# Performance work log

Hardware: AMD Instinct MI355X
Metric: run time of the kernel (lower is better)

## Reference

```python
import jax, jax.numpy as jnp
import numpy as np

M_STEP = 3  # model_args.m_step
E_STEP = 3  # model_args.e_step


def setup_inputs() -> dict:
    key = jax.random.key(0)
    ks = jax.random.split(key, 8)
    B, N, F = 1024, 11, 512   # batch, num_nodes (=round_id+2), message_size
    H = 512                   # link_hidden_size
    sc = 1.0 / np.sqrt(F)
    rnd = lambda k, shape: (jax.random.normal(k, shape, jnp.float32) * sc)
    return {
        "node_features": jax.random.normal(ks[0], (B, N, F), jnp.float32),
        "W1": rnd(ks[1], (H, F)),
        "b1": jnp.zeros((H,), jnp.float32),
        "W2": rnd(ks[2], (H, H)),
        "b2": jnp.zeros((H,), jnp.float32),
        "w_out": rnd(ks[3], (H,)),
        "b_out": jnp.zeros((), jnp.float32),
        "W_ih": rnd(ks[4], (3 * F, F)),  # GRU input weights (r,z,n), bias=False
        "W_hh": rnd(ks[5], (3 * F, F)),  # GRU hidden weights
    }


def _link_adj(x, W1, b1, W2, b2, w_out, b_out):
    # LinkFunction('graphconvattn'): pairwise node-feature interactions -> 1x1 conv stack -> [B,N,N]
    # x: [B,F,N]
    e = x[:, :, :, None] * x[:, :, None, :]                                  # [B,F,N,N]
    h = jax.nn.relu(jnp.einsum('bfij,gf->bgij', e, W1) + b1[None, :, None, None])
    h = jax.nn.relu(jnp.einsum('bfij,gf->bgij', h, W2) + b2[None, :, None, None])
    return jnp.einsum('bfij,f->bij', h, w_out) + b_out                       # [B,N,N]


def _gru_cell(m, h, W_ih, W_hh):
    # torch nn.GRU cell, bias=False, gate order (r, z, n)
    gi = m @ W_ih.T
    gh = h @ W_hh.T
    ir, iz, inn = jnp.split(gi, 3, axis=-1)
    hr, hz, hn = jnp.split(gh, 3, axis=-1)
    r = jax.nn.sigmoid(ir + hr)
    z = jax.nn.sigmoid(iz + hz)
    n = jnp.tanh(inn + r * hn)
    return (1.0 - z) * n + z * h


def reference(node_features, W1, b1, W2, b2, w_out, b_out, W_ih, W_hh):
    x0 = jnp.transpose(node_features, (0, 2, 1))   # [B,F,N]
    N = x0.shape[2]
    zidx = N - 1                                   # only the question node is updated
    col = x0[:, :, zidx]
    adj = None
    for t in range(M_STEP):
        # pred_node_feats[t]: original features with node z replaced by latest estimate
        pred = x0.at[:, :, zidx].set(col)
        adj = _link_adj(pred, W1, b1, W2, b2, w_out, b_out)
        A = jax.nn.softmax(adj, axis=2)            # softmax over neighbors
        a_z = A[:, zidx, :]                        # [B,N]
        h = pred
        for s in range(E_STEP):
            m_z = jnp.einsum('bj,bfj->bf', a_z, h)             # weighted message
            h_z = _gru_cell(m_z, h[:, :, zidx], W_ih, W_hh)    # GRU update
            h = h.at[:, :, zidx].set(h_z)
        col = h[:, :, zidx]
    # returns (pred_adj_mat from last m-step, final feature of node z)
    return adj, col
```

## Files before the change

kernel.cpp:

```cpp
#include <hip/hip_runtime.h>
#include <hip/hip_bf16.h>
#include <math.h>

#define Bsz 1024
#define Nn  11
#define Ff  512
#define Zi  10
#define G3  1536

#define PEC 65

typedef __attribute__((ext_vector_type(8))) short bfrag;
typedef __attribute__((ext_vector_type(4))) float f32x4;

__device__ __forceinline__ unsigned f2bf(float f) {
    __hip_bfloat16 h = __float2bfloat16(f);
    return (unsigned)*reinterpret_cast<unsigned short*>(&h);
}
__device__ __forceinline__ uint4 pack8(float v0, float v1, float v2, float v3,
                                       float v4, float v5, float v6, float v7) {
    uint4 pk;
    pk.x = f2bf(v0) | (f2bf(v1) << 16);
    pk.y = f2bf(v2) | (f2bf(v3) << 16);
    pk.z = f2bf(v4) | (f2bf(v5) << 16);
    pk.w = f2bf(v6) | (f2bf(v7) << 16);
    return pk;
}
__device__ __forceinline__ void pair_decode(int mode, int p, int& pi, int& pj) {
    if (mode == 0) { int r = p, i = 0; while (r >= Nn - i) { r -= Nn - i; ++i; } pi = i; pj = i + r; }
    else { pi = p; pj = Zi; }
}
__device__ __forceinline__ void gl_lds16(const void* src, void* dst) {
    __builtin_amdgcn_global_load_lds((const __attribute__((address_space(1))) void*)src,
                                     (__attribute__((address_space(3))) void*)dst, 16, 0, 0);
}

__global__ void init_col_kernel(const float* __restrict__ nf, float* __restrict__ col) {
    int idx = blockIdx.x * 256 + threadIdx.x;
    int b = idx >> 9, f = idx & 511;
    col[idx] = nf[(b * Nn + Zi) * Ff + f];
}

__global__ void pack_w_kernel(const float* __restrict__ src,
                              unsigned short* __restrict__ dst, int lgBW) {
    int idx = blockIdx.x * 256 + threadIdx.x;
    int g = idx >> 6, kq = idx & 63;
    int nb = g >> lgBW, gl = g & ((1 << lgBW) - 1);
    const float* s = src + g * Ff + kq * 8;
    float4 a = *(const float4*)s, b = *(const float4*)(s + 4);
    uint4 pk = pack8(a.x, a.y, a.z, a.w, b.x, b.y, b.z, b.w);
    long long dc = (((long long)(nb << 6) + kq) << lgBW) + gl;
    *(uint4*)((char*)dst + dc * 16) = pk;
}

__global__ __launch_bounds__(512, 2) void link_kernel(
    const float* __restrict__ nf, const float* __restrict__ colp,
    const unsigned short* __restrict__ W1p, const float* __restrict__ b1,
    const unsigned short* __restrict__ W2p, const float* __restrict__ b2,
    const float* __restrict__ w_out, const float* __restrict__ b_out,
    float* __restrict__ adj, int mode)
{
    __shared__ __align__(16) char Eb[64 * PEC * 16];
    __shared__ float Pl[8][64];

    const int tid = threadIdx.x;
    const int pr  = blockIdx.x >> 4;
    const int bc  = blockIdx.x & 15;
    int pi, pj; pair_decode(mode, pr, pi, pj);

    const int wid  = tid >> 6;
    const int l    = tid & 63;
    const int lr16 = l & 15;
    const int kq4  = l >> 4;

    const bfrag* W1c = (const bfrag*)W1p;
    const bfrag* W2c = (const bfrag*)W2p;
    const int wcb = wid * 64 + lr16;

    bfrag wb0[4], wb1[4];
    auto loadW = [&](int gs, bfrag* dst) {
        const bfrag* Wc = (gs >= 16) ? W2c : W1c;
        const int base = ((gs & 15) * 4 + kq4) * 512 + wcb;
#pragma unroll
        for (int nt = 0; nt < 4; ++nt) dst[nt] = Wc[base + nt * 16];
    };

    loadW(0, wb0);

    {
        const int row = tid >> 3;
        const int kc  = tid & 7;
        const int b   = bc * 64 + row;
        const float* xi = (pi == Zi) ? (colp + b * Ff) : (nf + (b * Nn + pi) * Ff);
        const float* xj = (pj == Zi) ? (colp + b * Ff) : (nf + (b * Nn + pj) * Ff);
#pragma unroll
        for (int i = 0; i < 8; ++i) {
            const int k0 = kc * 64 + i * 8;
            const int plane = k0 >> 3;
            float4 u0 = *(const float4*)(xi + k0), u1 = *(const float4*)(xi + k0 + 4);
            float4 v0 = *(const float4*)(xj + k0), v1 = *(const float4*)(xj + k0 + 4);
            *(uint4*)(&Eb[(plane * PEC + row) * 16]) =
                pack8(u0.x*v0.x, u0.y*v0.y, u0.z*v0.z, u0.w*v0.w,
                      u1.x*v1.x, u1.y*v1.y, u1.z*v1.z, u1.w*v1.w);
        }
    }
    __syncthreads();

    f32x4 acc[4][4];
#pragma unroll
    for (int mt = 0; mt < 4; ++mt)
#pragma unroll
        for (int nt = 0; nt < 4; ++nt) acc[mt][nt] = (f32x4){0.f, 0.f, 0.f, 0.f};

#define DO_STEP(S, WB) { \
    const int ebase = ((S) & 15) * 4 + kq4; \
    bfrag a0 = *(const bfrag*)(&Eb[(ebase * PEC +      lr16) * 16]); \
    bfrag a1 = *(const bfrag*)(&Eb[(ebase * PEC + 16 + lr16) * 16]); \
    bfrag a2 = *(const bfrag*)(&Eb[(ebase * PEC + 32 + lr16) * 16]); \
    bfrag a3 = *(const bfrag*)(&Eb[(ebase * PEC + 48 + lr16) * 16]); \
    acc[0][0] = __builtin_amdgcn_mfma_f32_16x16x32_bf16(a0, WB[0], acc[0][0], 0, 0, 0); \
    acc[0][1] = __builtin_amdgcn_mfma_f32_16x16x32_bf16(a0, WB[1], acc[0][1], 0, 0, 0); \
    acc[0][2] = __builtin_amdgcn_mfma_f32_16x16x32_bf16(a0, WB[2], acc[0][2], 0, 0, 0); \
    acc[0][3] = __builtin_amdgcn_mfma_f32_16x16x32_bf16(a0, WB[3], acc[0][3], 0, 0, 0); \
    acc[1][0] = __builtin_amdgcn_mfma_f32_16x16x32_bf16(a1, WB[0], acc[1][0], 0, 0, 0); \
    acc[1][1] = __builtin_amdgcn_mfma_f32_16x16x32_bf16(a1, WB[1], acc[1][1], 0, 0, 0); \
    acc[1][2] = __builtin_amdgcn_mfma_f32_16x16x32_bf16(a1, WB[2], acc[1][2], 0, 0, 0); \
    acc[1][3] = __builtin_amdgcn_mfma_f32_16x16x32_bf16(a1, WB[3], acc[1][3], 0, 0, 0); \
    acc[2][0] = __builtin_amdgcn_mfma_f32_16x16x32_bf16(a2, WB[0], acc[2][0], 0, 0, 0); \
    acc[2][1] = __builtin_amdgcn_mfma_f32_16x16x32_bf16(a2, WB[1], acc[2][1], 0, 0, 0); \
    acc[2][2] = __builtin_amdgcn_mfma_f32_16x16x32_bf16(a2, WB[2], acc[2][2], 0, 0, 0); \
    acc[2][3] = __builtin_amdgcn_mfma_f32_16x16x32_bf16(a2, WB[3], acc[2][3], 0, 0, 0); \
    acc[3][0] = __builtin_amdgcn_mfma_f32_16x16x32_bf16(a3, WB[0], acc[3][0], 0, 0, 0); \
    acc[3][1] = __builtin_amdgcn_mfma_f32_16x16x32_bf16(a3, WB[1], acc[3][1], 0, 0, 0); \
    acc[3][2] = __builtin_amdgcn_mfma_f32_16x16x32_bf16(a3, WB[2], acc[3][2], 0, 0, 0); \
    acc[3][3] = __builtin_amdgcn_mfma_f32_16x16x32_bf16(a3, WB[3], acc[3][3], 0, 0, 0); }

#pragma unroll 1
    for (int s2 = 0; s2 < 8; ++s2) {
        const int s = 2 * s2;
        loadW(s + 1, wb1);
        DO_STEP(s, wb0)
        loadW(s + 2, wb0);
        DO_STEP(s + 1, wb1)
    }

    __syncthreads();
    {
#pragma unroll
        for (int nt = 0; nt < 4; ++nt) {
            const int c  = wid * 64 + nt * 16 + lr16;
            const float bv = b1[c];
#pragma unroll
            for (int mt = 0; mt < 4; ++mt)
#pragma unroll
                for (int reg = 0; reg < 4; ++reg) {
                    int row = mt * 16 + kq4 * 4 + reg;
                    float v = fmaxf(acc[mt][nt][reg] + bv, 0.f);
                    *(unsigned short*)(&Eb[((c >> 3) * PEC + row) * 16 + (c & 7) * 2]) =
                        (unsigned short)f2bf(v);
                }
        }
#pragma unroll
        for (int mt = 0; mt < 4; ++mt)
#pragma unroll
            for (int nt = 0; nt < 4; ++nt) acc[mt][nt] = (f32x4){0.f, 0.f, 0.f, 0.f};
    }
    __syncthreads();

#pragma unroll 1
    for (int s2 = 0; s2 < 8; ++s2) {
        const int s = 16 + 2 * s2;
        loadW(s + 1, wb1);
        DO_STEP(s, wb0)
        if (s2 < 7) loadW(s + 2, wb0);
        DO_STEP(s + 1, wb1)
    }
#undef DO_STEP

    {
        float rs[4][4];
#pragma unroll
        for (int mt = 0; mt < 4; ++mt)
#pragma unroll
            for (int reg = 0; reg < 4; ++reg) rs[mt][reg] = 0.f;
#pragma unroll
        for (int nt = 0; nt < 4; ++nt) {
            const int c  = wid * 64 + nt * 16 + lr16;
            const float bv = b2[c];
            const float wv = w_out[c];
#pragma unroll
            for (int mt = 0; mt < 4; ++mt)
#pragma unroll
                for (int reg = 0; reg < 4; ++reg)
                    rs[mt][reg] += fmaxf(acc[mt][nt][reg] + bv, 0.f) * wv;
        }
#pragma unroll
        for (int off = 1; off < 16; off <<= 1)
#pragma unroll
            for (int mt = 0; mt < 4; ++mt)
#pragma unroll
                for (int reg = 0; reg < 4; ++reg)
                    rs[mt][reg] += __shfl_xor(rs[mt][reg], off);
        if (lr16 == 0) {
#pragma unroll
            for (int mt = 0; mt < 4; ++mt)
#pragma unroll
                for (int reg = 0; reg < 4; ++reg) {
                    int row = mt * 16 + kq4 * 4 + reg;
                    Pl[wid][row] = rs[mt][reg];
                }
        }
    }
    __syncthreads();
    if (tid < 64) {
        float v = b_out[0];
#pragma unroll
        for (int w = 0; w < 8; ++w) v += Pl[w][tid];
        int b = bc * 64 + tid;
        adj[b * (Nn * Nn) + pi * Nn + pj] = v;
        if (pi != pj) adj[b * (Nn * Nn) + pj * Nn + pi] = v;
    }
}

__global__ void softmax_az_kernel(const float* __restrict__ adj, float* __restrict__ a_z) {
    int b = blockIdx.x * 256 + threadIdx.x;
    if (b >= Bsz) return;
    const float* row = adj + b * (Nn * Nn) + Zi * Nn;
    float mx = row[0];
#pragma unroll
    for (int j = 1; j < Nn; ++j) mx = fmaxf(mx, row[j]);
    float e[Nn]; float s = 0.f;
#pragma unroll
    for (int j = 0; j < Nn; ++j) { e[j] = expf(row[j] - mx); s += e[j]; }
    float inv = 1.f / s;
#pragma unroll
    for (int j = 0; j < Nn; ++j) a_z[b * Nn + j] = e[j] * inv;
}

__global__ void mzpack_kernel(const float* __restrict__ nf, const float* __restrict__ a_z,
                              const float* __restrict__ col,
                              unsigned short* __restrict__ m_zp,
                              unsigned short* __restrict__ colbf) {
    int idx = blockIdx.x * 256 + threadIdx.x;
    int b = idx >> 6, kq = idx & 63;
    const float* az = a_z + b * Nn;
    const int f0 = kq * 8;
    float4 c0 = *(const float4*)(col + b * Ff + f0);
    float4 c1 = *(const float4*)(col + b * Ff + f0 + 4);
    float az10 = az[Zi];
    float s0 = az10 * c0.x, s1 = az10 * c0.y, s2 = az10 * c0.z, s3 = az10 * c0.w;
    float s4 = az10 * c1.x, s5 = az10 * c1.y, s6 = az10 * c1.z, s7 = az10 * c1.w;
#pragma unroll
    for (int j = 0; j < Nn - 1; ++j) {
        float aj = az[j];
        const float* p = nf + (b * Nn + j) * Ff + f0;
        float4 n0 = *(const float4*)p, n1 = *(const float4*)(p + 4);
        s0 += aj * n0.x; s1 += aj * n0.y; s2 += aj * n0.z; s3 += aj * n0.w;
        s4 += aj * n1.x; s5 += aj * n1.y; s6 += aj * n1.z; s7 += aj * n1.w;
    }
    long long dc = (((long long)(b >> 6) * 64 + kq) << 6) + (b & 63);
    *(uint4*)((char*)m_zp + dc * 16)  = pack8(s0, s1, s2, s3, s4, s5, s6, s7);
    *(uint4*)((char*)colbf + dc * 16) = pack8(c0.x, c0.y, c0.z, c0.w, c1.x, c1.y, c1.z, c1.w);
}

__global__ __launch_bounds__(256, 2) void gates_kernel(
    const unsigned short* __restrict__ m_zp, const unsigned short* __restrict__ colbf,
    const unsigned short* __restrict__ Wihp, const unsigned short* __restrict__ Whhp,
    float* __restrict__ gi, float* __restrict__ gh)
{
    __shared__ __align__(16) char Ab[64 * 64 * 16];

    const int xb = blockIdx.x, bc = blockIdx.y, tid = threadIdx.x;
    const bool isGi = xb < 6;
    const int nbase = (isGi ? xb : xb - 6) * 256;
    const unsigned short* Ap = isGi ? m_zp : colbf;
    const unsigned short* Wp = isGi ? Wihp : Whhp;
    float* C = isGi ? gi : gh;

    const int wid  = tid >> 6;
    const int l    = tid & 63;
    const int lr16 = l & 15;
    const int kq4  = l >> 4;

    const bfrag* Wc = (const bfrag*)Wp;
    const int wcb = ((nbase >> 9) << 15) + (nbase & 511) + wid * 64 + lr16;

    bfrag wb0[4], wb1[4];
    auto loadW = [&](int s, bfrag* dst) {
        const int base = wcb + (s * 4 + kq4) * 512;
#pragma unroll
        for (int nt = 0; nt < 4; ++nt) dst[nt] = Wc[base + nt * 16];
    };

    loadW(0, wb0);

#pragma unroll
    for (int i = 0; i < 16; ++i) {
        int cb = i * 256 + wid * 64;
        gl_lds16(Ap + ((long long)bc * 4096 + cb + l) * 8, (char*)Ab + cb * 16);
    }
    __syncthreads();

    f32x4 acc[4][4];
#pragma unroll
    for (int mt = 0; mt < 4; ++mt)
#pragma unroll
        for (int nt = 0; nt < 4; ++nt) acc[mt][nt] = (f32x4){0.f, 0.f, 0.f, 0.f};

#define DO_STEPG(S, WB) { \
    const int ebase = (S) * 4 + kq4; \
    bfrag a0 = *(const bfrag*)(&Ab[(ebase * 64 +      lr16) * 16]); \
    bfrag a1 = *(const bfrag*)(&Ab[(ebase * 64 + 16 + lr16) * 16]); \
    bfrag a2 = *(const bfrag*)(&Ab[(ebase * 64 + 32 + lr16) * 16]); \
    bfrag a3 = *(const bfrag*)(&Ab[(ebase * 64 + 48 + lr16) * 16]); \
    acc[0][0] = __builtin_amdgcn_mfma_f32_16x16x32_bf16(a0, WB[0], acc[0][0], 0, 0, 0); \
    acc[0][1] = __builtin_amdgcn_mfma_f32_16x16x32_bf16(a0, WB[1], acc[0][1], 0, 0, 0); \
    acc[0][2] = __builtin_amdgcn_mfma_f32_16x16x32_bf16(a0, WB[2], acc[0][2], 0, 0, 0); \
    acc[0][3] = __builtin_amdgcn_mfma_f32_16x16x32_bf16(a0, WB[3], acc[0][3], 0, 0, 0); \
    acc[1][0] = __builtin_amdgcn_mfma_f32_16x16x32_bf16(a1, WB[0], acc[1][0], 0, 0, 0); \
    acc[1][1] = __builtin_amdgcn_mfma_f32_16x16x32_bf16(a1, WB[1], acc[1][1], 0, 0, 0); \
    acc[1][2] = __builtin_amdgcn_mfma_f32_16x16x32_bf16(a1, WB[2], acc[1][2], 0, 0, 0); \
    acc[1][3] = __builtin_amdgcn_mfma_f32_16x16x32_bf16(a1, WB[3], acc[1][3], 0, 0, 0); \
    acc[2][0] = __builtin_amdgcn_mfma_f32_16x16x32_bf16(a2, WB[0], acc[2][0], 0, 0, 0); \
    acc[2][1] = __builtin_amdgcn_mfma_f32_16x16x32_bf16(a2, WB[1], acc[2][1], 0, 0, 0); \
    acc[2][2] = __builtin_amdgcn_mfma_f32_16x16x32_bf16(a2, WB[2], acc[2][2], 0, 0, 0); \
    acc[2][3] = __builtin_amdgcn_mfma_f32_16x16x32_bf16(a2, WB[3], acc[2][3], 0, 0, 0); \
    acc[3][0] = __builtin_amdgcn_mfma_f32_16x16x32_bf16(a3, WB[0], acc[3][0], 0, 0, 0); \
    acc[3][1] = __builtin_amdgcn_mfma_f32_16x16x32_bf16(a3, WB[1], acc[3][1], 0, 0, 0); \
    acc[3][2] = __builtin_amdgcn_mfma_f32_16x16x32_bf16(a3, WB[2], acc[3][2], 0, 0, 0); \
    acc[3][3] = __builtin_amdgcn_mfma_f32_16x16x32_bf16(a3, WB[3], acc[3][3], 0, 0, 0); }

#pragma unroll 1
    for (int s2 = 0; s2 < 8; ++s2) {
        const int s = 2 * s2;
        loadW(s + 1, wb1);
        DO_STEPG(s, wb0)
        if (s2 < 7) loadW(s + 2, wb0);
        DO_STEPG(s + 1, wb1)
    }
#undef DO_STEPG

#pragma unroll
    for (int nt = 0; nt < 4; ++nt) {
        const int c = nbase + wid * 64 + nt * 16 + lr16;
#pragma unroll
        for (int mt = 0; mt < 4; ++mt)
#pragma unroll
            for (int reg = 0; reg < 4; ++reg) {
                int row = mt * 16 + kq4 * 4 + reg;
                C[(bc * 64 + row) * G3 + c] = acc[mt][nt][reg];
            }
    }
}

__global__ void gru_kernel(const float* __restrict__ gi, const float* __restrict__ gh,
                           float* __restrict__ col) {
    int idx = blockIdx.x * 256 + threadIdx.x;
    int b = idx >> 7, f = (idx & 127) * 4;
    const float* gib = gi + b * G3;
    const float* ghb = gh + b * G3;
    float4 ir = *(const float4*)(gib + f);
    float4 iz = *(const float4*)(gib + Ff + f);
    float4 in = *(const float4*)(gib + 2 * Ff + f);
    float4 hr = *(const float4*)(ghb + f);
    float4 hz = *(const float4*)(ghb + Ff + f);
    float4 hn = *(const float4*)(ghb + 2 * Ff + f);
    float4 h  = *(const float4*)(col + b * Ff + f);
    float4 o;
#define GRU1(c) { \
    float r = 1.f / (1.f + expf(-(ir.c + hr.c))); \
    float z = 1.f / (1.f + expf(-(iz.c + hz.c))); \
    float n = tanhf(in.c + r * hn.c); \
    o.c = (1.f - z) * n + z * h.c; }
    GRU1(x) GRU1(y) GRU1(z) GRU1(w)
#undef GRU1
    *(float4*)(col + b * Ff + f) = o;
}

extern "C" void kernel_launch(void* const* d_in, const int* in_sizes, int n_in,
                              void* d_out, int out_size, void* d_ws, size_t ws_size,
                              hipStream_t stream) {
    const float* nf    = (const float*)d_in[0];
    const float* W1    = (const float*)d_in[1];
    const float* b1    = (const float*)d_in[2];
    const float* W2    = (const float*)d_in[3];
    const float* b2    = (const float*)d_in[4];
    const float* w_out = (const float*)d_in[5];
    const float* b_out = (const float*)d_in[6];
    const float* W_ih  = (const float*)d_in[7];
    const float* W_hh  = (const float*)d_in[8];

    float* adj = (float*)d_out;
    float* col = adj + Bsz * Nn * Nn;

    unsigned short* W1p   = (unsigned short*)d_ws;
    unsigned short* W2p   = W1p + Ff * Ff;
    unsigned short* Wihp  = W2p + Ff * Ff;
    unsigned short* Whhp  = Wihp + G3 * Ff;
    float* a_z            = (float*)(Whhp + G3 * Ff);
    unsigned short* m_zp  = (unsigned short*)(a_z + 16384);
    unsigned short* colbf = m_zp + Bsz * Ff;
    float* gi             = (float*)(colbf + Bsz * Ff);
    float* gh             = gi + Bsz * G3;

    init_col_kernel<<<(Bsz * Ff) / 256, 256, 0, stream>>>(nf, col);
    pack_w_kernel<<<(Ff * 64) / 256, 256, 0, stream>>>(W1, W1p, 9);
    pack_w_kernel<<<(Ff * 64) / 256, 256, 0, stream>>>(W2, W2p, 9);
    pack_w_kernel<<<(G3 * 64) / 256, 256, 0, stream>>>(W_ih, Wihp, 9);
    pack_w_kernel<<<(G3 * 64) / 256, 256, 0, stream>>>(W_hh, Whhp, 9);

    for (int t = 0; t < 3; ++t) {
        const int mode   = (t == 0) ? 0 : 1;
        const int npairs = (t == 0) ? 66 : 11;

        link_kernel<<<npairs * 16, 512, 0, stream>>>(nf, col, W1p, b1, W2p, b2,
                                                     w_out, b_out, adj, mode);
        softmax_az_kernel<<<Bsz / 256, 256, 0, stream>>>(adj, a_z);

        for (int s = 0; s < 3; ++s) {
            mzpack_kernel<<<(Bsz * 64) / 256, 256, 0, stream>>>(nf, a_z, col, m_zp, colbf);
            gates_kernel<<<dim3(12, 16), 256, 0, stream>>>(m_zp, colbf, Wihp, Whhp, gi, gh);
            gru_kernel<<<(Bsz * Ff) / 4 / 256, 256, 0, stream>>>(gi, gh, col);
        }
    }
}
```

Before: 364.4 us.

## Double link-kernel batch tile to 128 rows and triple-buffer gates weight loads

The link kernel now processes 128 batch rows per block instead of 64, so each loaded weight fragment feeds twice as many MFMAs and the grid is halved. This doubles accumulator registers and LDS use, and the launch bound of two blocks per SM may cause spills. The gates kernel gets padded LDS rows (PEC) to reduce bank conflicts and a three-deep weight prefetch rotation. A W2 prefetch is also moved out of the phase boundary, with weight indices clamped.

After: 435.7 us. 19.6% more time.

```diff
diff --git a/kernel.cpp b/kernel.cpp
--- a/kernel.cpp
+++ b/kernel.cpp
@@ -8,7 +8,8 @@
 #define Zi  10
 #define G3  1536
 
-#define PEC 65
+#define PEC  66
+#define PEL  130
 
 typedef __attribute__((ext_vector_type(8))) short bfrag;
 typedef __attribute__((ext_vector_type(4))) float f32x4;
@@ -60,12 +61,12 @@
     const float* __restrict__ w_out, const float* __restrict__ b_out,
     float* __restrict__ adj, int mode)
 {
-    __shared__ __align__(16) char Eb[64 * PEC * 16];
-    __shared__ float Pl[8][64];
+    __shared__ __align__(16) char Eb[64 * PEL * 16];
+    __shared__ float Pl[8][128];
 
     const int tid = threadIdx.x;
-    const int pr  = blockIdx.x >> 4;
-    const int bc  = blockIdx.x & 15;
+    const int pr  = blockIdx.x >> 3;
+    const int bc  = blockIdx.x & 7;
     int pi, pj; pair_decode(mode, pr, pi, pj);
 
     const int wid  = tid >> 6;
@@ -79,6 +80,7 @@
 
     bfrag wb0[4], wb1[4];
     auto loadW = [&](int gs, bfrag* dst) {
+        if (gs > 31) gs = 31;
         const bfrag* Wc = (gs >= 16) ? W2c : W1c;
         const int base = ((gs & 15) * 4 + kq4) * 512 + wcb;
 #pragma unroll
@@ -88,52 +90,40 @@
     loadW(0, wb0);
 
     {
-        const int row = tid >> 3;
-        const int kc  = tid & 7;
-        const int b   = bc * 64 + row;
+        const int row = tid >> 2;
+        const int kc  = tid & 3;
+        const int b   = bc * 128 + row;
         const float* xi = (pi == Zi) ? (colp + b * Ff) : (nf + (b * Nn + pi) * Ff);
         const float* xj = (pj == Zi) ? (colp + b * Ff) : (nf + (b * Nn + pj) * Ff);
 #pragma unroll
-        for (int i = 0; i < 8; ++i) {
-            const int k0 = kc * 64 + i * 8;
+        for (int i = 0; i < 16; ++i) {
+            const int k0 = kc * 128 + i * 8;
             const int plane = k0 >> 3;
             float4 u0 = *(const float4*)(xi + k0), u1 = *(const float4*)(xi + k0 + 4);
             float4 v0 = *(const float4*)(xj + k0), v1 = *(const float4*)(xj + k0 + 4);
-            *(uint4*)(&Eb[(plane * PEC + row) * 16]) =
+            *(uint4*)(&Eb[(plane * PEL + row) * 16]) =
                 pack8(u0.x*v0.x, u0.y*v0.y, u0.z*v0.z, u0.w*v0.w,
                       u1.x*v1.x, u1.y*v1.y, u1.z*v1.z, u1.w*v1.w);
         }
     }
     __syncthreads();
 
-    f32x4 acc[4][4];
-#pragma unroll
-    for (int mt = 0; mt < 4; ++mt)
+    f32x4 acc[8][4];
+#pragma unroll
+    for (int mt = 0; mt < 8; ++mt)
 #pragma unroll
         for (int nt = 0; nt < 4; ++nt) acc[mt][nt] = (f32x4){0.f, 0.f, 0.f, 0.f};
 
 #define DO_STEP(S, WB) { \
     const int ebase = ((S) & 15) * 4 + kq4; \
-    bfrag a0 = *(const bfrag*)(&Eb[(ebase * PEC +      lr16) * 16]); \
-    bfrag a1 = *(const bfrag*)(&Eb[(ebase * PEC + 16 + lr16) * 16]); \
-    bfrag a2 = *(const bfrag*)(&Eb[(ebase * PEC + 32 + lr16) * 16]); \
-    bfrag a3 = *(const bfrag*)(&Eb[(ebase * PEC + 48 + lr16) * 16]); \
-    acc[0][0] = __builtin_amdgcn_mfma_f32_16x16x32_bf16(a0, WB[0], acc[0][0], 0, 0, 0); \
-    acc[0][1] = __builtin_amdgcn_mfma_f32_16x16x32_bf16(a0, WB[1], acc[0][1], 0, 0, 0); \
-    acc[0][2] = __builtin_amdgcn_mfma_f32_16x16x32_bf16(a0, WB[2], acc[0][2], 0, 0, 0); \
-    acc[0][3] = __builtin_amdgcn_mfma_f32_16x16x32_bf16(a0, WB[3], acc[0][3], 0, 0, 0); \
-    acc[1][0] = __builtin_amdgcn_mfma_f32_16x16x32_bf16(a1, WB[0], acc[1][0], 0, 0, 0); \
-    acc[1][1] = __builtin_amdgcn_mfma_f32_16x16x32_bf16(a1, WB[1], acc[1][1], 0, 0, 0); \
-    acc[1][2] = __builtin_amdgcn_mfma_f32_16x16x32_bf16(a1, WB[2], acc[1][2], 0, 0, 0); \
-    acc[1][3] = __builtin_amdgcn_mfma_f32_16x16x32_bf16(a1, WB[3], acc[1][3], 0, 0, 0); \
-    acc[2][0] = __builtin_amdgcn_mfma_f32_16x16x32_bf16(a2, WB[0], acc[2][0], 0, 0, 0); \
-    acc[2][1] = __builtin_amdgcn_mfma_f32_16x16x32_bf16(a2, WB[1], acc[2][1], 0, 0, 0); \
-    acc[2][2] = __builtin_amdgcn_mfma_f32_16x16x32_bf16(a2, WB[2], acc[2][2], 0, 0, 0); \
-    acc[2][3] = __builtin_amdgcn_mfma_f32_16x16x32_bf16(a2, WB[3], acc[2][3], 0, 0, 0); \
-    acc[3][0] = __builtin_amdgcn_mfma_f32_16x16x32_bf16(a3, WB[0], acc[3][0], 0, 0, 0); \
-    acc[3][1] = __builtin_amdgcn_mfma_f32_16x16x32_bf16(a3, WB[1], acc[3][1], 0, 0, 0); \
-    acc[3][2] = __builtin_amdgcn_mfma_f32_16x16x32_bf16(a3, WB[2], acc[3][2], 0, 0, 0); \
-    acc[3][3] = __builtin_amdgcn_mfma_f32_16x16x32_bf16(a3, WB[3], acc[3][3], 0, 0, 0); }
+    _Pragma("unroll") \
+    for (int mt = 0; mt < 8; ++mt) { \
+        bfrag a = *(const bfrag*)(&Eb[(ebase * PEL + mt * 16 + lr16) * 16]); \
+        acc[mt][0] = __builtin_amdgcn_mfma_f32_16x16x32_bf16(a, WB[0], acc[mt][0], 0, 0, 0); \
+        acc[mt][1] = __builtin_amdgcn_mfma_f32_16x16x32_bf16(a, WB[1], acc[mt][1], 0, 0, 0); \
+        acc[mt][2] = __builtin_amdgcn_mfma_f32_16x16x32_bf16(a, WB[2], acc[mt][2], 0, 0, 0); \
+        acc[mt][3] = __builtin_amdgcn_mfma_f32_16x16x32_bf16(a, WB[3], acc[mt][3], 0, 0, 0); \
+    } }
 
 #pragma unroll 1
     for (int s2 = 0; s2 < 8; ++s2) {
@@ -151,36 +141,37 @@
             const int c  = wid * 64 + nt * 16 + lr16;
             const float bv = b1[c];
 #pragma unroll
-            for (int mt = 0; mt < 4; ++mt)
+            for (int mt = 0; mt < 8; ++mt)
 #pragma unroll
                 for (int reg = 0; reg < 4; ++reg) {
                     int row = mt * 16 + kq4 * 4 + reg;
                     float v = fmaxf(acc[mt][nt][reg] + bv, 0.f);
-                    *(unsigned short*)(&Eb[((c >> 3) * PEC + row) * 16 + (c & 7) * 2]) =
+                    *(unsigned short*)(&Eb[((c >> 3) * PEL + row) * 16 + (c & 7) * 2]) =
                         (unsigned short)f2bf(v);
                 }
         }
 #pragma unroll
-        for (int mt = 0; mt < 4; ++mt)
+        for (int mt = 0; mt < 8; ++mt)
 #pragma unroll
             for (int nt = 0; nt < 4; ++nt) acc[mt][nt] = (f32x4){0.f, 0.f, 0.f, 0.f};
     }
     __syncthreads();
 
+    loadW(16, wb0);
 #pragma unroll 1
     for (int s2 = 0; s2 < 8; ++s2) {
         const int s = 16 + 2 * s2;
         loadW(s + 1, wb1);
         DO_STEP(s, wb0)
-        if (s2 < 7) loadW(s + 2, wb0);
+        loadW(s + 2, wb0);
         DO_STEP(s + 1, wb1)
     }
 #undef DO_STEP
 
     {
-        float rs[4][4];
-#pragma unroll
-        for (int mt = 0; mt < 4; ++mt)
+        float rs[8][4];
+#pragma unroll
+        for (int mt = 0; mt < 8; ++mt)
 #pragma unroll
             for (int reg = 0; reg < 4; ++reg) rs[mt][reg] = 0.f;
 #pragma unroll
@@ -189,7 +180,7 @@
             const float bv = b2[c];
             const float wv = w_out[c];
 #pragma unroll
-            for (int mt = 0; mt < 4; ++mt)
+            for (int mt = 0; mt < 8; ++mt)
 #pragma unroll
                 for (int reg = 0; reg < 4; ++reg)
                     rs[mt][reg] += fmaxf(acc[mt][nt][reg] + bv, 0.f) * wv;
@@ -197,13 +188,13 @@
 #pragma unroll
         for (int off = 1; off < 16; off <<= 1)
 #pragma unroll
-            for (int mt = 0; mt < 4; ++mt)
+            for (int mt = 0; mt < 8; ++mt)
 #pragma unroll
                 for (int reg = 0; reg < 4; ++reg)
                     rs[mt][reg] += __shfl_xor(rs[mt][reg], off);
         if (lr16 == 0) {
 #pragma unroll
-            for (int mt = 0; mt < 4; ++mt)
+            for (int mt = 0; mt < 8; ++mt)
 #pragma unroll
                 for (int reg = 0; reg < 4; ++reg) {
                     int row = mt * 16 + kq4 * 4 + reg;
@@ -212,11 +203,11 @@
         }
     }
     __syncthreads();
-    if (tid < 64) {
+    if (tid < 128) {
         float v = b_out[0];
 #pragma unroll
         for (int w = 0; w < 8; ++w) v += Pl[w][tid];
-        int b = bc * 64 + tid;
+        int b = bc * 128 + tid;
         adj[b * (Nn * Nn) + pi * Nn + pj] = v;
         if (pi != pj) adj[b * (Nn * Nn) + pj * Nn + pi] = v;
     }
@@ -268,7 +259,7 @@
     const unsigned short* __restrict__ Wihp, const unsigned short* __restrict__ Whhp,
     float* __restrict__ gi, float* __restrict__ gh)
 {
-    __shared__ __align__(16) char Ab[64 * 64 * 16];
+    __shared__ __align__(16) char Ab[64 * PEC * 16];
 
     const int xb = blockIdx.x, bc = blockIdx.y, tid = threadIdx.x;
     const bool isGi = xb < 6;
@@ -285,19 +276,22 @@
     const bfrag* Wc = (const bfrag*)Wp;
     const int wcb = ((nbase >> 9) << 15) + (nbase & 511) + wid * 64 + lr16;
 
-    bfrag wb0[4], wb1[4];
+    bfrag wbA[4], wbB[4], wbC[4];
     auto loadW = [&](int s, bfrag* dst) {
+        if (s > 15) s = 15;
         const int base = wcb + (s * 4 + kq4) * 512;
 #pragma unroll
         for (int nt = 0; nt < 4; ++nt) dst[nt] = Wc[base + nt * 16];
     };
 
-    loadW(0, wb0);
+    loadW(0, wbA);
+    loadW(1, wbB);
 
 #pragma unroll
     for (int i = 0; i < 16; ++i) {
-        int cb = i * 256 + wid * 64;
-        gl_lds16(Ap + ((long long)bc * 4096 + cb + l) * 8, (char*)Ab + cb * 16);
+        const int p = i * 4 + wid;
+        gl_lds16(Ap + ((long long)bc * 4096 + p * 64 + l) * 8,
+                 (char*)Ab + (p * PEC) * 16);
     }
     __syncthreads();
 
@@ -309,35 +303,23 @@
 
 #define DO_STEPG(S, WB) { \
     const int ebase = (S) * 4 + kq4; \
-    bfrag a0 = *(const bfrag*)(&Ab[(ebase * 64 +      lr16) * 16]); \
-    bfrag a1 = *(const bfrag*)(&Ab[(ebase * 64 + 16 + lr16) * 16]); \
-    bfrag a2 = *(const bfrag*)(&Ab[(ebase * 64 + 32 + lr16) * 16]); \
-    bfrag a3 = *(const bfrag*)(&Ab[(ebase * 64 + 48 + lr16) * 16]); \
-    acc[0][0] = __builtin_amdgcn_mfma_f32_16x16x32_bf16(a0, WB[0], acc[0][0], 0, 0, 0); \
-    acc[0][1] = __builtin_amdgcn_mfma_f32_16x16x32_bf16(a0, WB[1], acc[0][1], 0, 0, 0); \
-    acc[0][2] = __builtin_amdgcn_mfma_f32_16x16x32_bf16(a0, WB[2], acc[0][2], 0, 0, 0); \
-    acc[0][3] = __builtin_amdgcn_mfma_f32_16x16x32_bf16(a0, WB[3], acc[0][3], 0, 0, 0); \
-    acc[1][0] = __builtin_amdgcn_mfma_f32_16x16x32_bf16(a1, WB[0], acc[1][0], 0, 0, 0); \
-    acc[1][1] = __builtin_amdgcn_mfma_f32_16x16x32_bf16(a1, WB[1], acc[1][1], 0, 0, 0); \
-    acc[1][2] = __builtin_amdgcn_mfma_f32_16x16x32_bf16(a1, WB[2], acc[1][2], 0, 0, 0); \
-    acc[1][3] = __builtin_amdgcn_mfma_f32_16x16x32_bf16(a1, WB[3], acc[1][3], 0, 0, 0); \
-    acc[2][0] = __builtin_amdgcn_mfma_f32_16x16x32_bf16(a2, WB[0], acc[2][0], 0, 0, 0); \
-    acc[2][1] = __builtin_amdgcn_mfma_f32_16x16x32_bf16(a2, WB[1], acc[2][1], 0, 0, 0); \
-    acc[2][2] = __builtin_amdgcn_mfma_f32_16x16x32_bf16(a2, WB[2], acc[2][2], 0, 0, 0); \
-    acc[2][3] = __builtin_amdgcn_mfma_f32_16x16x32_bf16(a2, WB[3], acc[2][3], 0, 0, 0); \
-    acc[3][0] = __builtin_amdgcn_mfma_f32_16x16x32_bf16(a3, WB[0], acc[3][0], 0, 0, 0); \
-    acc[3][1] = __builtin_amdgcn_mfma_f32_16x16x32_bf16(a3, WB[1], acc[3][1], 0, 0, 0); \
-    acc[3][2] = __builtin_amdgcn_mfma_f32_16x16x32_bf16(a3, WB[2], acc[3][2], 0, 0, 0); \
-    acc[3][3] = __builtin_amdgcn_mfma_f32_16x16x32_bf16(a3, WB[3], acc[3][3], 0, 0, 0); }
+    _Pragma("unroll") \
+    for (int mt = 0; mt < 4; ++mt) { \
+        bfrag a = *(const bfrag*)(&Ab[(ebase * PEC + mt * 16 + lr16) * 16]); \
+        acc[mt][0] = __builtin_amdgcn_mfma_f32_16x16x32_bf16(a, WB[0], acc[mt][0], 0, 0, 0); \
+        acc[mt][1] = __builtin_amdgcn_mfma_f32_16x16x32_bf16(a, WB[1], acc[mt][1], 0, 0, 0); \
+        acc[mt][2] = __builtin_amdgcn_mfma_f32_16x16x32_bf16(a, WB[2], acc[mt][2], 0, 0, 0); \
+        acc[mt][3] = __builtin_amdgcn_mfma_f32_16x16x32_bf16(a, WB[3], acc[mt][3], 0, 0, 0); \
+    } }
 
 #pragma unroll 1
-    for (int s2 = 0; s2 < 8; ++s2) {
-        const int s = 2 * s2;
-        loadW(s + 1, wb1);
-        DO_STEPG(s, wb0)
-        if (s2 < 7) loadW(s + 2, wb0);
-        DO_STEPG(s + 1, wb1)
-    }
+    for (int i = 0; i < 5; ++i) {
+        const int s = 3 * i;
+        loadW(s + 2, wbC); DO_STEPG(s,     wbA)
+        loadW(s + 3, wbA); DO_STEPG(s + 1, wbB)
+        loadW(s + 4, wbB); DO_STEPG(s + 2, wbC)
+    }
+    DO_STEPG(15, wbA)
 #undef DO_STEPG
 
 #pragma unroll
@@ -413,8 +395,8 @@
         const int mode   = (t == 0) ? 0 : 1;
         const int npairs = (t == 0) ? 66 : 11;
 
-        link_kernel<<<npairs * 16, 512, 0, stream>>>(nf, col, W1p, b1, W2p, b2,
-                                                     w_out, b_out, adj, mode);
+        link_kernel<<<npairs * 8, 512, 0, stream>>>(nf, col, W1p, b1, W2p, b2,
+                                                    w_out, b_out, adj, mode);
         softmax_az_kernel<<<Bsz / 256, 256, 0, stream>>>(adj, a_z);
 
         for (int s = 0; s < 3; ++s) {
```

## Hoist fixed-neighbor message GEMM out of GRU loop and concatenate gate weights

Applied to the files above, without the earlier changes.

Splits m_z into a fixed part from the non-updated nodes plus a_z10*h. The fixed part's input-gate GEMM is computed once per m-step and stored as bf16. Each e-step then runs one GEMM of h against the concatenated [W_ih; W_hh], and the GRU kernel adds az10*(W_ih h). The GRU kernel also writes the packed bf16 column directly, which removes the separate m_z pack kernel per e-step. The tradeoff is extra bf16 rounding of the fixed gate contribution and a 3072-wide output buffer.

Result: slower. 443.8 us (+21.8%).

```diff
diff --git a/kernel.cpp b/kernel.cpp
--- a/kernel.cpp
+++ b/kernel.cpp
@@ -16,6 +16,11 @@
 __device__ __forceinline__ unsigned f2bf(float f) {
     __hip_bfloat16 h = __float2bfloat16(f);
     return (unsigned)*reinterpret_cast<unsigned short*>(&h);
+}
+__device__ __forceinline__ float bf2f(unsigned short u) {
+    union { unsigned int i; float f; } v;
+    v.i = ((unsigned int)u) << 16;
+    return v.f;
 }
 __device__ __forceinline__ uint4 pack8(float v0, float v1, float v2, float v3,
                                        float v4, float v5, float v6, float v7) {
@@ -35,21 +40,28 @@
                                      (__attribute__((address_space(3))) void*)dst, 16, 0, 0);
 }
 
-__global__ void init_col_kernel(const float* __restrict__ nf, float* __restrict__ col) {
+__global__ void init_col2_kernel(const float* __restrict__ nf, float* __restrict__ col,
+                                 unsigned short* __restrict__ colbf) {
     int idx = blockIdx.x * 256 + threadIdx.x;
-    int b = idx >> 9, f = idx & 511;
-    col[idx] = nf[(b * Nn + Zi) * Ff + f];
+    int b = idx >> 6, kq = idx & 63;
+    const float* s = nf + (b * Nn + Zi) * Ff + kq * 8;
+    float4 a = *(const float4*)s, c = *(const float4*)(s + 4);
+    *(float4*)(col + b * Ff + kq * 8)     = a;
+    *(float4*)(col + b * Ff + kq * 8 + 4) = c;
+    long long dc = (((long long)(b >> 6) * 64 + kq) << 6) + (b & 63);
+    *(uint4*)((char*)colbf + dc * 16) = pack8(a.x, a.y, a.z, a.w, c.x, c.y, c.z, c.w);
 }
 
 __global__ void pack_w_kernel(const float* __restrict__ src,
-                              unsigned short* __restrict__ dst, int lgBW) {
+                              unsigned short* __restrict__ dst, int lgBW, int goff) {
     int idx = blockIdx.x * 256 + threadIdx.x;
-    int g = idx >> 6, kq = idx & 63;
-    int nb = g >> lgBW, gl = g & ((1 << lgBW) - 1);
-    const float* s = src + g * Ff + kq * 8;
+    int gl_ = idx >> 6, kq = idx & 63;
+    int g = gl_ + goff;
+    int nb = g >> lgBW, gg = g & ((1 << lgBW) - 1);
+    const float* s = src + gl_ * Ff + kq * 8;
     float4 a = *(const float4*)s, b = *(const float4*)(s + 4);
     uint4 pk = pack8(a.x, a.y, a.z, a.w, b.x, b.y, b.z, b.w);
-    long long dc = (((long long)(nb << 6) + kq) << lgBW) + gl;
+    long long dc = (((long long)(nb << 6) + kq) << lgBW) + gg;
     *(uint4*)((char*)dst + dc * 16) = pk;
 }
 
@@ -237,19 +249,13 @@
     for (int j = 0; j < Nn; ++j) a_z[b * Nn + j] = e[j] * inv;
 }
 
-__global__ void mzpack_kernel(const float* __restrict__ nf, const float* __restrict__ a_z,
-                              const float* __restrict__ col,
-                              unsigned short* __restrict__ m_zp,
-                              unsigned short* __restrict__ colbf) {
+__global__ void mfixpack_kernel(const float* __restrict__ nf, const float* __restrict__ a_z,
+                                unsigned short* __restrict__ m_fixp) {
     int idx = blockIdx.x * 256 + threadIdx.x;
     int b = idx >> 6, kq = idx & 63;
     const float* az = a_z + b * Nn;
     const int f0 = kq * 8;
-    float4 c0 = *(const float4*)(col + b * Ff + f0);
-    float4 c1 = *(const float4*)(col + b * Ff + f0 + 4);
-    float az10 = az[Zi];
-    float s0 = az10 * c0.x, s1 = az10 * c0.y, s2 = az10 * c0.z, s3 = az10 * c0.w;
-    float s4 = az10 * c1.x, s5 = az10 * c1.y, s6 = az10 * c1.z, s7 = az10 * c1.w;
+    float s0 = 0.f, s1 = 0.f, s2 = 0.f, s3 = 0.f, s4 = 0.f, s5 = 0.f, s6 = 0.f, s7 = 0.f;
 #pragma unroll
     for (int j = 0; j < Nn - 1; ++j) {
         float aj = az[j];
@@ -259,87 +265,74 @@
         s4 += aj * n1.x; s5 += aj * n1.y; s6 += aj * n1.z; s7 += aj * n1.w;
     }
     long long dc = (((long long)(b >> 6) * 64 + kq) << 6) + (b & 63);
-    *(uint4*)((char*)m_zp + dc * 16)  = pack8(s0, s1, s2, s3, s4, s5, s6, s7);
-    *(uint4*)((char*)colbf + dc * 16) = pack8(c0.x, c0.y, c0.z, c0.w, c1.x, c1.y, c1.z, c1.w);
-}
-
-__global__ __launch_bounds__(256, 2) void gates_kernel(
-    const unsigned short* __restrict__ m_zp, const unsigned short* __restrict__ colbf,
-    const unsigned short* __restrict__ Wihp, const unsigned short* __restrict__ Whhp,
-    float* __restrict__ gi, float* __restrict__ gh)
+    *(uint4*)((char*)m_fixp + dc * 16) = pack8(s0, s1, s2, s3, s4, s5, s6, s7);
+}
+
+#define GEMM_CORE                                                              \
+    __shared__ __align__(16) char Ab[64 * 64 * 16];                            \
+    const int xb = blockIdx.x, bc = blockIdx.y, tid = threadIdx.x;             \
+    const int nbase = xb * 256;                                                \
+    const int wid  = tid >> 6;                                                 \
+    const int l    = tid & 63;                                                 \
+    const int lr16 = l & 15;                                                   \
+    const int kq4  = l >> 4;                                                   \
+    const bfrag* Wc = (const bfrag*)Wp;                                        \
+    const int wcb = ((nbase >> 9) << 15) + (nbase & 511) + wid * 64 + lr16;    \
+    bfrag wb0[4], wb1[4];                                                      \
+    auto loadW = [&](int s, bfrag* dst) {                                      \
+        if (s > 15) s = 15;                                                    \
+        const int base = wcb + (s * 4 + kq4) * 512;                            \
+        _Pragma("unroll")                                                      \
+        for (int nt = 0; nt < 4; ++nt) dst[nt] = Wc[base + nt * 16];           \
+    };                                                                         \
+    loadW(0, wb0);                                                             \
+    _Pragma("unroll")                                                          \
+    for (int i = 0; i < 16; ++i) {                                             \
+        int cb = i * 256 + wid * 64;                                           \
+        gl_lds16(Ap + ((long long)bc * 4096 + cb + l) * 8, (char*)Ab + cb * 16); \
+    }                                                                          \
+    __syncthreads();                                                           \
+    f32x4 acc[4][4];                                                           \
+    _Pragma("unroll")                                                          \
+    for (int mt = 0; mt < 4; ++mt)                                             \
+        _Pragma("unroll")                                                      \
+        for (int nt = 0; nt < 4; ++nt) acc[mt][nt] = (f32x4){0.f, 0.f, 0.f, 0.f}; \
+    _Pragma("unroll 1")                                                        \
+    for (int s2 = 0; s2 < 8; ++s2) {                                           \
+        const int s = 2 * s2;                                                  \
+        loadW(s + 1, wb1);                                                     \
+        { const int ebase = s * 4 + kq4;                                       \
+          bfrag a0 = *(const bfrag*)(&Ab[(ebase * 64 +      lr16) * 16]);      \
+          bfrag a1 = *(const bfrag*)(&Ab[(ebase * 64 + 16 + lr16) * 16]);      \
+          bfrag a2 = *(const bfrag*)(&Ab[(ebase * 64 + 32 + lr16) * 16]);      \
+          bfrag a3 = *(const bfrag*)(&Ab[(ebase * 64 + 48 + lr16) * 16]);      \
+          _Pragma("unroll")                                                    \
+          for (int nt = 0; nt < 4; ++nt) {                                     \
+            acc[0][nt] = __builtin_amdgcn_mfma_f32_16x16x32_bf16(a0, wb0[nt], acc[0][nt], 0, 0, 0); \
+            acc[1][nt] = __builtin_amdgcn_mfma_f32_16x16x32_bf16(a1, wb0[nt], acc[1][nt], 0, 0, 0); \
+            acc[2][nt] = __builtin_amdgcn_mfma_f32_16x16x32_bf16(a2, wb0[nt], acc[2][nt], 0, 0, 0); \
+            acc[3][nt] = __builtin_amdgcn_mfma_f32_16x16x32_bf16(a3, wb0[nt], acc[3][nt], 0, 0, 0); \
+          } }                                                                  \
+        loadW(s + 2, wb0);                                                     \
+        { const int ebase = (s + 1) * 4 + kq4;                                 \
+          bfrag a0 = *(const bfrag*)(&Ab[(ebase * 64 +      lr16) * 16]);      \
+          bfrag a1 = *(const bfrag*)(&Ab[(ebase * 64 + 16 + lr16) * 16]);      \
+          bfrag a2 = *(const bfrag*)(&Ab[(ebase * 64 + 32 + lr16) * 16]);      \
+          bfrag a3 = *(const bfrag*)(&Ab[(ebase * 64 + 48 + lr16) * 16]);      \
+          _Pragma("unroll")                                                    \
+          for (int nt = 0; nt < 4; ++nt) {                                     \
+            acc[0][nt] = __builtin_amdgcn_mfma_f32_16x16x32_bf16(a0, wb1[nt], acc[0][nt], 0, 0, 0); \
+            acc[1][nt] = __builtin_amdgcn_mfma_f32_16x16x32_bf16(a1, wb1[nt], acc[1][nt], 0, 0, 0); \
+            acc[2][nt] = __builtin_amdgcn_mfma_f32_16x16x32_bf16(a2, wb1[nt], acc[2][nt], 0, 0, 0); \
+            acc[3][nt] = __builtin_amdgcn_mfma_f32_16x16x32_bf16(a3, wb1[nt], acc[3][nt], 0, 0, 0); \
+          } }                                                                  \
+    }
+
+__global__ __launch_bounds__(256, 2) void gifix_kernel(
+    const unsigned short* __restrict__ Ap, const unsigned short* __restrict__ Wp,
+    unsigned short* __restrict__ Cout)
 {
-    __shared__ __align__(16) char Ab[64 * 64 * 16];
-
-    const int xb = blockIdx.x, bc = blockIdx.y, tid = threadIdx.x;
-    const bool isGi = xb < 6;
-    const int nbase = (isGi ? xb : xb - 6) * 256;
-    const unsigned short* Ap = isGi ? m_zp : colbf;
-    const unsigned short* Wp = isGi ? Wihp : Whhp;
-    float* C = isGi ? gi : gh;
-
-    const int wid  = tid >> 6;
-    const int l    = tid & 63;
-    const int lr16 = l & 15;
-    const int kq4  = l >> 4;
-
-    const bfrag* Wc = (const bfrag*)Wp;
-    const int wcb = ((nbase >> 9) << 15) + (nbase & 511) + wid * 64 + lr16;
-
-    bfrag wb0[4], wb1[4];
-    auto loadW = [&](int s, bfrag* dst) {
-        const int base = wcb + (s * 4 + kq4) * 512;
-#pragma unroll
-        for (int nt = 0; nt < 4; ++nt) dst[nt] = Wc[base + nt * 16];
-    };
-
-    loadW(0, wb0);
-
-#pragma unroll
-    for (int i = 0; i < 16; ++i) {
-        int cb = i * 256 + wid * 64;
-        gl_lds16(Ap + ((long long)bc * 4096 + cb + l) * 8, (char*)Ab + cb * 16);
-    }
-    __syncthreads();
-
-    f32x4 acc[4][4];
-#pragma unroll
-    for (int mt = 0; mt < 4; ++mt)
-#pragma unroll
-        for (int nt = 0; nt < 4; ++nt) acc[mt][nt] = (f32x4){0.f, 0.f, 0.f, 0.f};
-
-#define DO_STEPG(S, WB) { \
-    const int ebase = (S) * 4 + kq4; \
-    bfrag a0 = *(const bfrag*)(&Ab[(ebase * 64 +      lr16) * 16]); \
-    bfrag a1 = *(const bfrag*)(&Ab[(ebase * 64 + 16 + lr16) * 16]); \
-    bfrag a2 = *(const bfrag*)(&Ab[(ebase * 64 + 32 + lr16) * 16]); \
-    bfrag a3 = *(const bfrag*)(&Ab[(ebase * 64 + 48 + lr16) * 16]); \
-    acc[0][0] = __builtin_amdgcn_mfma_f32_16x16x32_bf16(a0, WB[0], acc[0][0], 0, 0, 0); \
-    acc[0][1] = __builtin_amdgcn_mfma_f32_16x16x32_bf16(a0, WB[1], acc[0][1], 0, 0, 0); \
-    acc[0][2] = __builtin_amdgcn_mfma_f32_16x16x32_bf16(a0, WB[2], acc[0][2], 0, 0, 0); \
-    acc[0][3] = __builtin_amdgcn_mfma_f32_16x16x32_bf16(a0, WB[3], acc[0][3], 0, 0, 0); \
-    acc[1][0] = __builtin_amdgcn_mfma_f32_16x16x32_bf16(a1, WB[0], acc[1][0], 0, 0, 0); \
-    acc[1][1] = __builtin_amdgcn_mfma_f32_16x16x32_bf16(a1, WB[1], acc[1][1], 0, 0, 0); \
-    acc[1][2] = __builtin_amdgcn_mfma_f32_16x16x32_bf16(a1, WB[2], acc[1][2], 0, 0, 0); \
-    acc[1][3] = __builtin_amdgcn_mfma_f32_16x16x32_bf16(a1, WB[3], acc[1][3], 0, 0, 0); \
-    acc[2][0] = __builtin_amdgcn_mfma_f32_16x16x32_bf16(a2, WB[0], acc[2][0], 0, 0, 0); \
-    acc[2][1] = __builtin_amdgcn_mfma_f32_16x16x32_bf16(a2, WB[1], acc[2][1], 0, 0, 0); \
-    acc[2][2] = __builtin_amdgcn_mfma_f32_16x16x32_bf16(a2, WB[2], acc[2][2], 0, 0, 0); \
-    acc[2][3] = __builtin_amdgcn_mfma_f32_16x16x32_bf16(a2, WB[3], acc[2][3], 0, 0, 0); \
-    acc[3][0] = __builtin_amdgcn_mfma_f32_16x16x32_bf16(a3, WB[0], acc[3][0], 0, 0, 0); \
-    acc[3][1] = __builtin_amdgcn_mfma_f32_16x16x32_bf16(a3, WB[1], acc[3][1], 0, 0, 0); \
-    acc[3][2] = __builtin_amdgcn_mfma_f32_16x16x32_bf16(a3, WB[2], acc[3][2], 0, 0, 0); \
-    acc[3][3] = __builtin_amdgcn_mfma_f32_16x16x32_bf16(a3, WB[3], acc[3][3], 0, 0, 0); }
-
-#pragma unroll 1
-    for (int s2 = 0; s2 < 8; ++s2) {
-        const int s = 2 * s2;
-        loadW(s + 1, wb1);
-        DO_STEPG(s, wb0)
-        if (s2 < 7) loadW(s + 2, wb0);
-        DO_STEPG(s + 1, wb1)
-    }
-#undef DO_STEPG
-
+    GEMM_CORE
 #pragma unroll
     for (int nt = 0; nt < 4; ++nt) {
         const int c = nbase + wid * 64 + nt * 16 + lr16;
@@ -348,33 +341,60 @@
 #pragma unroll
             for (int reg = 0; reg < 4; ++reg) {
                 int row = mt * 16 + kq4 * 4 + reg;
-                C[(bc * 64 + row) * G3 + c] = acc[mt][nt][reg];
+                Cout[(bc * 64 + row) * G3 + c] = (unsigned short)f2bf(acc[mt][nt][reg]);
             }
     }
 }
 
-__global__ void gru_kernel(const float* __restrict__ gi, const float* __restrict__ gh,
-                           float* __restrict__ col) {
+__global__ __launch_bounds__(256, 2) void gatescat_kernel(
+    const unsigned short* __restrict__ Ap, const unsigned short* __restrict__ Wp,
+    float* __restrict__ Cout)
+{
+    GEMM_CORE
+#pragma unroll
+    for (int nt = 0; nt < 4; ++nt) {
+        const int c = nbase + wid * 64 + nt * 16 + lr16;
+#pragma unroll
+        for (int mt = 0; mt < 4; ++mt)
+#pragma unroll
+            for (int reg = 0; reg < 4; ++reg) {
+                int row = mt * 16 + kq4 * 4 + reg;
+                Cout[(bc * 64 + row) * 3072 + c] = acc[mt][nt][reg];
+            }
+    }
+}
+
+__global__ void gru2_kernel(const unsigned short* __restrict__ gifixb,
+                            const float* __restrict__ C3,
+                            const float* __restrict__ a_z,
+                            float* __restrict__ col,
+                            unsigned short* __restrict__ colbf) {
     int idx = blockIdx.x * 256 + threadIdx.x;
-    int b = idx >> 7, f = (idx & 127) * 4;
-    const float* gib = gi + b * G3;
-    const float* ghb = gh + b * G3;
-    float4 ir = *(const float4*)(gib + f);
-    float4 iz = *(const float4*)(gib + Ff + f);
-    float4 in = *(const float4*)(gib + 2 * Ff + f);
-    float4 hr = *(const float4*)(ghb + f);
-    float4 hz = *(const float4*)(ghb + Ff + f);
-    float4 hn = *(const float4*)(ghb + 2 * Ff + f);
-    float4 h  = *(const float4*)(col + b * Ff + f);
-    float4 o;
-#define GRU1(c) { \
-    float r = 1.f / (1.f + expf(-(ir.c + hr.c))); \
-    float z = 1.f / (1.f + expf(-(iz.c + hz.c))); \
-    float n = tanhf(in.c + r * hn.c); \
-    o.c = (1.f - z) * n + z * h.c; }
-    GRU1(x) GRU1(y) GRU1(z) GRU1(w)
-#undef GRU1
-    *(float4*)(col + b * Ff + f) = o;
+    int b = idx >> 6, kq = idx & 63;
+    const int f0 = kq * 8;
+    const float az10 = a_z[b * Nn + Zi];
+    const float* u  = C3 + (long long)b * 3072;
+    const float* hh = u + G3;
+    const unsigned short* gf = gifixb + (long long)b * G3;
+
+    float o[8];
+#pragma unroll
+    for (int k = 0; k < 8; ++k) {
+        int f = f0 + k;
+        float ir = bf2f(gf[f])        + az10 * u[f];
+        float iz = bf2f(gf[512 + f])  + az10 * u[512 + f];
+        float in = bf2f(gf[1024 + f]) + az10 * u[1024 + f];
+        float hr = hh[f], hz = hh[512 + f], hn = hh[1024 + f];
+        float r = 1.f / (1.f + expf(-(ir + hr)));
+        float z = 1.f / (1.f + expf(-(iz + hz)));
+        float n = tanhf(in + r * hn);
+        float h = col[b * Ff + f];
+        o[k] = (1.f - z) * n + z * h;
+    }
+    *(float4*)(col + b * Ff + f0)     = (float4){o[0], o[1], o[2], o[3]};
+    *(float4*)(col + b * Ff + f0 + 4) = (float4){o[4], o[5], o[6], o[7]};
+    long long dc = (((long long)(b >> 6) * 64 + kq) << 6) + (b & 63);
+    *(uint4*)((char*)colbf + dc * 16) = pack8(o[0], o[1], o[2], o[3], o[4], o[5], o[6], o[7]);
 }
 
 extern "C" void kernel_launch(void* const* d_in, const int* in_sizes, int n_in,
@@ -393,21 +413,20 @@
     float* adj = (float*)d_out;
     float* col = adj + Bsz * Nn * Nn;
 
-    unsigned short* W1p   = (unsigned short*)d_ws;
-    unsigned short* W2p   = W1p + Ff * Ff;
-    unsigned short* Wihp  = W2p + Ff * Ff;
-    unsigned short* Whhp  = Wihp + G3 * Ff;
-    float* a_z            = (float*)(Whhp + G3 * Ff);
-    unsigned short* m_zp  = (unsigned short*)(a_z + 16384);
-    unsigned short* colbf = m_zp + Bsz * Ff;
-    float* gi             = (float*)(colbf + Bsz * Ff);
-    float* gh             = gi + Bsz * G3;
-
-    init_col_kernel<<<(Bsz * Ff) / 256, 256, 0, stream>>>(nf, col);
-    pack_w_kernel<<<(Ff * 64) / 256, 256, 0, stream>>>(W1, W1p, 9);
-    pack_w_kernel<<<(Ff * 64) / 256, 256, 0, stream>>>(W2, W2p, 9);
-    pack_w_kernel<<<(G3 * 64) / 256, 256, 0, stream>>>(W_ih, Wihp, 9);
-    pack_w_kernel<<<(G3 * 64) / 256, 256, 0, stream>>>(W_hh, Whhp, 9);
+    unsigned short* W1p    = (unsigned short*)d_ws;
+    unsigned short* W2p    = W1p + Ff * Ff;
+    unsigned short* Wcatp  = W2p + Ff * Ff;
+    float* a_z             = (float*)(Wcatp + 2 * G3 * Ff);
+    unsigned short* colbf  = (unsigned short*)(a_z + 16384);
+    unsigned short* gifixb = colbf + Bsz * Ff;
+    float* C3              = (float*)(gifixb + (long long)Bsz * G3);
+    unsigned short* m_fixp = (unsigned short*)C3;
+
+    init_col2_kernel<<<(Bsz * 64) / 256, 256, 0, stream>>>(nf, col, colbf);
+    pack_w_kernel<<<(Ff * 64) / 256, 256, 0, stream>>>(W1, W1p, 9, 0);
+    pack_w_kernel<<<(Ff * 64) / 256, 256, 0, stream>>>(W2, W2p, 9, 0);
+    pack_w_kernel<<<(G3 * 64) / 256, 256, 0, stream>>>(W_ih, Wcatp, 9, 0);
+    pack_w_kernel<<<(G3 * 64) / 256, 256, 0, stream>>>(W_hh, Wcatp, 9, G3);
 
     for (int t = 0; t < 3; ++t) {
         const int mode   = (t == 0) ? 0 : 1;
@@ -416,11 +435,12 @@
         link_kernel<<<npairs * 16, 512, 0, stream>>>(nf, col, W1p, b1, W2p, b2,
                                                      w_out, b_out, adj, mode);
         softmax_az_kernel<<<Bsz / 256, 256, 0, stream>>>(adj, a_z);
+        mfixpack_kernel<<<(Bsz * 64) / 256, 256, 0, stream>>>(nf, a_z, m_fixp);
+        gifix_kernel<<<dim3(6, 16), 256, 0, stream>>>(m_fixp, Wcatp, gifixb);
 
         for (int s = 0; s < 3; ++s) {
-            mzpack_kernel<<<(Bsz * 64) / 256, 256, 0, stream>>>(nf, a_z, col, m_zp, colbf);
-            gates_kernel<<<dim3(12, 16), 256, 0, stream>>>(m_zp, colbf, Wihp, Whhp, gi, gh);
-            gru_kernel<<<(Bsz * Ff) / 4 / 256, 256, 0, stream>>>(gi, gh, col);
+            gatescat_kernel<<<dim3(12, 16), 256, 0, stream>>>(colbf, Wcatp, C3);
+            gru2_kernel<<<(Bsz * 64) / 256, 256, 0, stream>>>(gifixb, C3, a_z, col, colbf);
         }
     }
 }
```
